# Optimization experiments

Hardware: AMD Instinct MI355X
Metric: run time of the kernel (lower is better)

Reference implementation:

```python
import jax, jax.numpy as jnp
import numpy as np

B, S, H, NH = 4, 2048, 768, 12
HD = H // NH

def _ln(x, g, b, eps=1e-5):
    m = jnp.mean(x, -1, keepdims=True)
    v = jnp.mean((x - m) ** 2, -1, keepdims=True)
    return (x - m) * jax.lax.rsqrt(v + eps) * g + b

def setup_inputs() -> dict:
    key = jax.random.key(0)
    ks = jax.random.split(key, 16)
    s = 0.02
    return {
        "x": jax.random.normal(ks[0], (B, S, H), jnp.float32),
        "prev_state": jax.random.normal(ks[1], (B, S, H), jnp.float32),
        "mask": jax.random.randint(ks[2], (B,), 0, 2).astype(bool),
        # depthwise conv1d (groups=H, k=3): torch weight [H, 1, 3] == OIH
        "conv_dw_w": jax.random.normal(ks[3], (H, 1, 3), jnp.float32) * s,
        "conv_dw_b": jnp.zeros((H,), jnp.float32),
        # pointwise conv1d (k=1) stored as [out, in]
        "conv_pw_w": jax.random.normal(ks[4], (H, H), jnp.float32) * s,
        "conv_pw_b": jnp.zeros((H,), jnp.float32),
        "cn_g": jnp.ones((H,), jnp.float32), "cn_b": jnp.zeros((H,), jnp.float32),
        "Wq": jax.random.normal(ks[5], (H, H), jnp.float32) * s, "bq": jnp.zeros((H,), jnp.float32),
        "Wk": jax.random.normal(ks[6], (H, H), jnp.float32) * s, "bk": jnp.zeros((H,), jnp.float32),
        "Wv": jax.random.normal(ks[7], (H, H), jnp.float32) * s, "bv": jnp.zeros((H,), jnp.float32),
        "Wo": jax.random.normal(ks[8], (H, H), jnp.float32) * s, "bo": jnp.zeros((H,), jnp.float32),
        "pn_g": jnp.ones((H,), jnp.float32), "pn_b": jnp.zeros((H,), jnp.float32),
        "Wpost": jax.random.normal(ks[9], (H, H), jnp.float32) * s, "bpost": jnp.zeros((H,), jnp.float32),
        "Wg": jax.random.normal(ks[10], (1, 2 * H), jnp.float32) * s, "bg": jnp.zeros((1,), jnp.float32),
    }

def reference(x, prev_state, mask, conv_dw_w, conv_dw_b, conv_pw_w, conv_pw_b,
              cn_g, cn_b, Wq, bq, Wk, bk, Wv, bv, Wo, bo,
              pn_g, pn_b, Wpost, bpost, Wg, bg):
    # ---- bridge: depthwise conv (k=3) -> pointwise conv (k=1) -> GELU -> LN ----
    mem_t = prev_state.transpose(0, 2, 1)  # [B, H, S]
    dw = jax.lax.conv_general_dilated(
        mem_t, conv_dw_w, window_strides=(1,), padding=[(1, 1)],
        feature_group_count=H, dimension_numbers=("NCH", "OIH", "NCH")) + conv_dw_b[None, :, None]
    pw = jnp.einsum("bhs,oh->bos", dw, conv_pw_w) + conv_pw_b[None, :, None]
    bridged = jax.nn.gelu(pw, approximate=False).transpose(0, 2, 1)  # [B, S, H]
    bridged = _ln(bridged, cn_g, cn_b)
    # ---- cross attention: q from x, k/v from bridged memory (nope, non-causal) ----
    q = (jnp.einsum("bsh,oh->bso", x, Wq) + bq).reshape(B, S, NH, HD)
    k = (jnp.einsum("bsh,oh->bso", bridged, Wk) + bk).reshape(B, S, NH, HD)
    v = (jnp.einsum("bsh,oh->bso", bridged, Wv) + bv).reshape(B, S, NH, HD)
    scores = jnp.einsum("bqnd,bknd->bnqk", q, k) / np.float32(np.sqrt(HD))
    attn = jax.nn.softmax(scores, axis=-1)
    ao = jnp.einsum("bnqk,bknd->bqnd", attn, v).reshape(B, S, H)
    ao = jnp.einsum("bsh,oh->bso", ao, Wo) + bo
    # ---- post-attn norm, linear, gate, scatter-add back under mask ----
    inj = _ln(ao, pn_g, pn_b)
    inj = jnp.einsum("bsh,oh->bso", inj, Wpost) + bpost
    gate = jax.nn.sigmoid(jnp.einsum("bsh,oh->bso", jnp.concatenate([x, bridged], -1), Wg) + bg)
    gated = gate * jnp.tanh(inj)
    mf = mask.astype(x.dtype)[:, None, None]  # batch-row select == masked scatter-add
    out = x + mf * gated
    # masked MSE aux loss (only over selected rows, as in the original)
    denom = jnp.maximum(mask.sum(), 1).astype(x.dtype) * np.float32(S * H)
    aux = jnp.sum(mf * (bridged - x) ** 2) / denom
    return out, aux
```

## Files before the change

kernel.cpp:

```cpp
#include <hip/hip_runtime.h>
#include <math.h>

#define B_ 4
#define S_ 2048
#define H_ 768
#define NH_ 12
#define HD_ 64
#define BSH (B_ * S_ * H_)
#define NROWS (B_ * S_)
#define WSZ (H_ * H_)

typedef __attribute__((ext_vector_type(8))) short bf16x8;
typedef __attribute__((ext_vector_type(4))) short s16x4;
typedef __attribute__((ext_vector_type(4))) float f32x4;
typedef __attribute__((ext_vector_type(2))) unsigned u32x2;
typedef __attribute__((ext_vector_type(4))) unsigned u32x4;

__device__ __forceinline__ short f2bf(float f) {
  union { float f; unsigned u; } x; x.f = f;
  unsigned r = x.u + 0x7FFF + ((x.u >> 16) & 1);
  return (short)(r >> 16);
}
__device__ __forceinline__ float bf2f(short s) {
  union { unsigned u; float f; } x;
  x.u = ((unsigned)(unsigned short)s) << 16;
  return x.f;
}
__device__ __forceinline__ unsigned bfpack(float lo, float hi) {
  union { float f; unsigned u; } a, b; a.f = lo; b.f = hi;
  return __builtin_amdgcn_perm(b.u, a.u, 0x07060302);
}

__device__ __forceinline__ float fexp2(float x) {
#if __has_builtin(__builtin_amdgcn_exp2f)
  return __builtin_amdgcn_exp2f(x);
#else
  float r;
  asm("v_exp_f32 %0, %1" : "=v"(r) : "v"(x));
  return r;
#endif
}

__device__ __forceinline__ void plswap32(unsigned& a, unsigned& b) {
#if __has_builtin(__builtin_amdgcn_permlane32_swap)
  u32x2 r = __builtin_amdgcn_permlane32_swap(a, b, false, false);
  a = r.x; b = r.y;
#else
  asm volatile("v_permlane32_swap_b32 %0, %1" : "+v"(a), "+v"(b));
#endif
}
__device__ __forceinline__ void plswap16(unsigned& a, unsigned& b) {
#if __has_builtin(__builtin_amdgcn_permlane16_swap)
  u32x2 r = __builtin_amdgcn_permlane16_swap(a, b, false, false);
  a = r.x; b = r.y;
#else
  asm volatile("v_permlane16_swap_b32 %0, %1" : "+v"(a), "+v"(b));
#endif
}

typedef __attribute__((address_space(1))) const unsigned int g_u32;
typedef __attribute__((address_space(3))) unsigned int l_u32;
__device__ __forceinline__ void gload16(const void* g, void* l) {
  __builtin_amdgcn_global_load_lds((g_u32*)g, (l_u32*)l, 16, 0, 0);
}

__global__ __launch_bounds__(256) void cvt_x_k(const float* __restrict__ src,
                                               short* __restrict__ dst) {
  int i = (blockIdx.x * 256 + threadIdx.x) * 4;
  float4 v = *(const float4*)(src + i);
  s16x4 o = {f2bf(v.x), f2bf(v.y), f2bf(v.z), f2bf(v.w)};
  *(s16x4*)(dst + i) = o;
}

__global__ __launch_bounds__(256) void cvt6_k(const float* w0, const float* w1,
                                              const float* w2, const float* w3,
                                              const float* w4, const float* w5,
                                              short* __restrict__ dst) {
  int i = (blockIdx.x * 256 + threadIdx.x) * 4;
  int m = i / WSZ;
  int off = i - m * WSZ;
  const float* s = m == 0 ? w0 : m == 1 ? w1 : m == 2 ? w2 : m == 3 ? w3 : m == 4 ? w4 : w5;
  float sc = (m == 1) ? 0.1803368802f : 1.0f;
  float4 v = *(const float4*)(s + off);
  s16x4 o = {f2bf(v.x * sc), f2bf(v.y * sc), f2bf(v.z * sc), f2bf(v.w * sc)};
  *(s16x4*)(dst + i) = o;
}

__global__ __launch_bounds__(192) void dwconv_k(const float* __restrict__ prev,
                                                const float* __restrict__ w3,
                                                const float* __restrict__ bias,
                                                short* __restrict__ out) {
  int row = blockIdx.x;
  int s = row & (S_ - 1);
  int h = threadIdx.x * 4;
  size_t base = (size_t)row * H_ + h;
  float4 c = *(const float4*)(prev + base);
  float4 wa = *(const float4*)(w3 + h * 3);
  float4 wb = *(const float4*)(w3 + h * 3 + 4);
  float4 wc = *(const float4*)(w3 + h * 3 + 8);
  float4 bi = *(const float4*)(bias + h);
  float4 acc;
  acc.x = bi.x + c.x * wa.y;
  acc.y = bi.y + c.y * wb.x;
  acc.z = bi.z + c.z * wb.w;
  acc.w = bi.w + c.w * wc.z;
  if (s > 0) {
    float4 l = *(const float4*)(prev + base - H_);
    acc.x += l.x * wa.x; acc.y += l.y * wa.w; acc.z += l.z * wb.z; acc.w += l.w * wc.y;
  }
  if (s < S_ - 1) {
    float4 r = *(const float4*)(prev + base + H_);
    acc.x += r.x * wa.z; acc.y += r.y * wb.y; acc.z += r.z * wc.x; acc.w += r.w * wc.w;
  }
  s16x4 o = {f2bf(acc.x), f2bf(acc.y), f2bf(acc.z), f2bf(acc.w)};
  *(s16x4*)(out + base) = o;
}

struct GemmJob {
  const short* A; const short* W; const float* bias; short* C; int act; int tout;
  float bscale;
};

__global__ __launch_bounds__(256, 2) void gemm_bf2(GemmJob j0, GemmJob j1, GemmJob j2) {
  int d = blockIdx.x;
  int z = d / 384, r5 = d - z * 384;
  GemmJob j = z == 0 ? j0 : (z == 1 ? j1 : j2);
  int xcd = r5 & 7, s5 = r5 >> 3;
  int nx = s5 % 6, ny = xcd + 8 * (s5 / 6);
  __shared__ short As[3][128 * 64];
  __shared__ short Ws[2][128 * 64];
  int tid = threadIdx.x, lane = tid & 63, w = tid >> 6;
  int wr = w >> 1, wc = w & 1, lm = lane & 15, lq = lane >> 4;
  int lm7 = lm & 15 & 7;
  int rb8 = (lq ^ lm7) << 3, rb8x = rb8 ^ 32;
  int m0 = ny * 128, n0 = nx * 128;
  int srow = lane >> 3;
  int jl = ((lane & 7) ^ srow) * 8;
  const short* gA = j.A + (size_t)(m0 + w * 32 + srow) * H_ + jl;
  const short* gW = j.W + (size_t)(n0 + w * 32 + srow) * H_ + jl;
  int lbase = w * 2048;

  f32x4 acc[4][4];
#pragma unroll
  for (int i = 0; i < 4; ++i)
#pragma unroll
    for (int jj = 0; jj < 4; ++jj) acc[i][jj] = (f32x4){0.f, 0.f, 0.f, 0.f};

#pragma unroll
  for (int c = 0; c < 4; ++c)
    gload16(gA + (size_t)(c * 8) * H_, &As[0][lbase + c * 512]);
#pragma unroll
  for (int c = 0; c < 4; ++c)
    gload16(gW + (size_t)(c * 8) * H_, &Ws[0][lbase + c * 512]);
#pragma unroll
  for (int c = 0; c < 4; ++c)
    gload16(gA + 64 + (size_t)(c * 8) * H_, &As[1][lbase + c * 512]);

  const int NST = H_ / 64;
  for (int t = 0; t < NST; ++t) {
    if (t < NST - 1) asm volatile("s_waitcnt vmcnt(4)" ::: "memory");
    else             asm volatile("s_waitcnt vmcnt(0)" ::: "memory");
    __builtin_amdgcn_s_barrier();
    __builtin_amdgcn_sched_barrier(0);
    if (t + 1 < NST) {
      int kt1 = (t + 1) * 64;
#pragma unroll
      for (int c = 0; c < 4; ++c)
        gload16(gW + kt1 + (size_t)(c * 8) * H_, &Ws[(t + 1) & 1][lbase + c * 512]);
    }
    if (t + 2 < NST) {
      int kt2 = (t + 2) * 64;
      int a2 = (t + 2) % 3;
#pragma unroll
      for (int c = 0; c < 4; ++c)
        gload16(gA + kt2 + (size_t)(c * 8) * H_, &As[a2][lbase + c * 512]);
    }
    const short* Aw = &As[t % 3][0];
    const short* Ww = &Ws[t & 1][0];
#pragma unroll
    for (int kk = 0; kk < 2; ++kk) {
      int ro = kk ? rb8x : rb8;
      bf16x8 af[4], wf[4];
#pragma unroll
      for (int i = 0; i < 4; ++i)
        af[i] = *(const bf16x8*)&Aw[(wr * 64 + i * 16 + lm) * 64 + ro];
#pragma unroll
      for (int jj = 0; jj < 4; ++jj)
        wf[jj] = *(const bf16x8*)&Ww[(wc * 64 + jj * 16 + lm) * 64 + ro];
#pragma unroll
      for (int i = 0; i < 4; ++i)
#pragma unroll
        for (int jj = 0; jj < 4; ++jj)
          acc[i][jj] = __builtin_amdgcn_mfma_f32_16x16x32_bf16(af[i], wf[jj], acc[i][jj], 0, 0, 0);
    }
  }

  if (!j.tout) {
#pragma unroll
    for (int jj = 0; jj < 4; ++jj) {
      int col = n0 + wc * 64 + jj * 16 + lm;
      float bn = j.bias[col] * j.bscale;
#pragma unroll
      for (int i = 0; i < 4; ++i) {
        int mrow = m0 + wr * 64 + i * 16 + lq * 4;
#pragma unroll
        for (int r = 0; r < 4; ++r) {
          float cv = acc[i][jj][r] + bn;
          if (j.act) cv = 0.5f * cv * (1.0f + erff(cv * 0.70710678118f));
          j.C[(size_t)(mrow + r) * H_ + col] = f2bf(cv);
        }
      }
    }
  } else {
    int b = m0 >> 11;
    int sb = (m0 & (S_ - 1)) + wr * 64;
#pragma unroll
    for (int jj = 0; jj < 4; ++jj) {
      int col = n0 + wc * 64 + jj * 16 + lm;
      float bn = j.bias[col] * j.bscale;
      short* cp = j.C + ((size_t)(b * H_ + col)) * S_;
#pragma unroll
      for (int i = 0; i < 4; ++i) {
        int s = sb + i * 16 + lq * 4;
        s16x4 pk = {f2bf(acc[i][jj][0] + bn), f2bf(acc[i][jj][1] + bn),
                    f2bf(acc[i][jj][2] + bn), f2bf(acc[i][jj][3] + bn)};
        *(s16x4*)(cp + s) = pk;
      }
    }
  }
}

__global__ __launch_bounds__(256, 3) void gemm_n64(const short* __restrict__ A,
                                                   const short* __restrict__ W,
                                                   const float* __restrict__ bias,
                                                   short* __restrict__ C, int act) {
  int d = blockIdx.x;
  int xcd = d & 7, s5 = d >> 3;
  int nx = s5 % 12, ny = xcd + 8 * (s5 / 12);
  __shared__ short As[2][128 * 64];
  __shared__ short Ws[2][64 * 64];
  int tid = threadIdx.x, lane = tid & 63, w = tid >> 6;
  int wm = w >> 1, wn = w & 1, lm = lane & 15, lq = lane >> 4;
  int lm7 = lm & 7;
  int rb8 = (lq ^ lm7) << 3, rb8x = rb8 ^ 32;
  int m0 = ny * 128, n0 = nx * 64;
  int srow = lane >> 3;
  int jl = ((lane & 7) ^ srow) * 8;
  const short* gA = A + (size_t)(m0 + w * 32 + srow) * H_ + jl;
  const short* gW = W + (size_t)(n0 + w * 16 + srow) * H_ + jl;
  int lbaseA = w * 2048;
  int lbaseW = w * 1024;

  f32x4 acc[4][2];
#pragma unroll
  for (int i = 0; i < 4; ++i)
#pragma unroll
    for (int jj = 0; jj < 2; ++jj) acc[i][jj] = (f32x4){0.f, 0.f, 0.f, 0.f};

#pragma unroll
  for (int c = 0; c < 4; ++c)
    gload16(gA + (size_t)(c * 8) * H_, &As[0][lbaseA + c * 512]);
#pragma unroll
  for (int c = 0; c < 2; ++c)
    gload16(gW + (size_t)(c * 8) * H_, &Ws[0][lbaseW + c * 512]);

  for (int kt = 0, pb = 0; kt < H_; kt += 64, pb ^= 1) {
    __syncthreads();
    if (kt + 64 < H_) {
#pragma unroll
      for (int c = 0; c < 4; ++c)
        gload16(gA + kt + 64 + (size_t)(c * 8) * H_, &As[pb ^ 1][lbaseA + c * 512]);
#pragma unroll
      for (int c = 0; c < 2; ++c)
        gload16(gW + kt + 64 + (size_t)(c * 8) * H_, &Ws[pb ^ 1][lbaseW + c * 512]);
    }
    const short* Aw = &As[pb][0];
    const short* Ww = &Ws[pb][0];
#pragma unroll
    for (int kk = 0; kk < 2; ++kk) {
      int ro = kk ? rb8x : rb8;
      bf16x8 af[4], wf[2];
#pragma unroll
      for (int i = 0; i < 4; ++i)
        af[i] = *(const bf16x8*)&Aw[(wm * 64 + i * 16 + lm) * 64 + ro];
#pragma unroll
      for (int jj = 0; jj < 2; ++jj)
        wf[jj] = *(const bf16x8*)&Ww[(wn * 32 + jj * 16 + lm) * 64 + ro];
#pragma unroll
      for (int i = 0; i < 4; ++i)
#pragma unroll
        for (int jj = 0; jj < 2; ++jj)
          acc[i][jj] = __builtin_amdgcn_mfma_f32_16x16x32_bf16(af[i], wf[jj], acc[i][jj], 0, 0, 0);
    }
  }

#pragma unroll
  for (int jj = 0; jj < 2; ++jj) {
    int col = n0 + wn * 32 + jj * 16 + lm;
    float bn = bias[col];
#pragma unroll
    for (int i = 0; i < 4; ++i) {
      int mrow = m0 + wm * 64 + i * 16 + lq * 4;
#pragma unroll
      for (int r = 0; r < 4; ++r) {
        float cv = acc[i][jj][r] + bn;
        if (act) cv = 0.5f * cv * (1.0f + erff(cv * 0.70710678118f));
        C[(size_t)(mrow + r) * H_ + col] = f2bf(cv);
      }
    }
  }
}

__global__ __launch_bounds__(256) void ln_bf(const short* __restrict__ X,
                                             short* __restrict__ Y,
                                             const float* __restrict__ g,
                                             const float* __restrict__ bb) {
  int row = blockIdx.x;
  size_t base = (size_t)row * H_;
  int h0 = threadIdx.x, h1 = h0 + 256, h2 = h0 + 512;
  float x0 = bf2f(X[base + h0]), x1 = bf2f(X[base + h1]), x2 = bf2f(X[base + h2]);
  float s = x0 + x1 + x2;
  float s2 = x0 * x0 + x1 * x1 + x2 * x2;
  for (int off = 32; off > 0; off >>= 1) {
    s += __shfl_down(s, off);
    s2 += __shfl_down(s2, off);
  }
  __shared__ float sa[4], sq[4], st[2];
  int wid = threadIdx.x >> 6, lane = threadIdx.x & 63;
  if (lane == 0) { sa[wid] = s; sq[wid] = s2; }
  __syncthreads();
  if (threadIdx.x == 0) {
    float ts = sa[0] + sa[1] + sa[2] + sa[3];
    float ts2 = sq[0] + sq[1] + sq[2] + sq[3];
    float mean = ts * (1.0f / H_);
    float var = ts2 * (1.0f / H_) - mean * mean;
    st[0] = mean;
    st[1] = rsqrtf(var + 1e-5f);
  }
  __syncthreads();
  float mean = st[0], rstd = st[1];
  Y[base + h0] = f2bf((x0 - mean) * rstd * g[h0] + bb[h0]);
  Y[base + h1] = f2bf((x1 - mean) * rstd * g[h1] + bb[h1]);
  Y[base + h2] = f2bf((x2 - mean) * rstd * g[h2] + bb[h2]);
}

__global__ __launch_bounds__(256, 3) void attn8_k(const short* __restrict__ qb,
                                                  const short* __restrict__ kb,
                                                  const short* __restrict__ vtb,
                                                  short* __restrict__ aob) {
  __shared__ short Ks[2][64 * 64];
  __shared__ short Vt[2][64 * 64];
  int tid = threadIdx.x, lane = tid & 63, w = tid >> 6;
  int lm = lane & 15, lq = lane >> 4;
  int lm7 = lm & 7;
  int dd = blockIdx.x;
  int xcd = dd & 7, slot = dd >> 3;
  int g = xcd + 8 * (slot >> 4);
  int qx = slot & 15;
  int b = g / NH_, n = g - b * NH_;
  int q0 = qx * 128;
  int hoff = n * HD_;

  int rb8 = (lq ^ lm7) << 3;
  int rb8x = rb8 ^ 32;

  bf16x8 qf[2][2];
#pragma unroll
  for (int qg = 0; qg < 2; ++qg) {
    const short* qrow = qb + ((size_t)(b * S_ + q0 + w * 32 + qg * 16 + lm)) * H_ + hoff;
    qf[qg][0] = *(const bf16x8*)(qrow + lq * 8);
    qf[qg][1] = *(const bf16x8*)(qrow + 32 + lq * 8);
  }

  bf16x8 onef = {0x3F80, 0x3F80, 0x3F80, 0x3F80, 0x3F80, 0x3F80, 0x3F80, 0x3F80};
  f32x4 ls[2];
  ls[0] = (f32x4){0.f, 0.f, 0.f, 0.f};
  ls[1] = (f32x4){0.f, 0.f, 0.f, 0.f};

  f32x4 o[4][2];
#pragma unroll
  for (int i = 0; i < 4; ++i)
#pragma unroll
    for (int qg = 0; qg < 2; ++qg) o[i][qg] = (f32x4){0.f, 0.f, 0.f, 0.f};

  int jl = ((lane & 7) ^ (lane >> 3)) * 8;
  int rr = w * 16 + (lane >> 3);
  const short* kgl = kb + ((size_t)(b * S_ + rr)) * H_ + hoff + jl;
  const short* vgl = vtb + ((size_t)(b * H_ + hoff + rr)) * S_ + jl;
  int lbase = w * 1024;

#pragma unroll
  for (int c = 0; c < 2; ++c) {
    gload16(kgl + (size_t)(c * 8) * H_, &Ks[0][lbase + c * 512]);
    gload16(vgl + (size_t)(c * 8) * S_, &Vt[0][lbase + c * 512]);
  }

  for (int kt = 0, pb = 0; kt < S_; kt += 64, pb ^= 1) {
    __syncthreads();
    if (kt + 64 < S_) {
#pragma unroll
      for (int c = 0; c < 2; ++c) {
        gload16(kgl + (size_t)(kt + 64 + c * 8) * H_, &Ks[pb ^ 1][lbase + c * 512]);
        gload16(vgl + (size_t)(c * 8) * S_ + (kt + 64), &Vt[pb ^ 1][lbase + c * 512]);
      }
    }
    const short* Kw = &Ks[pb][0];
    const short* Vw = &Vt[pb][0];

    f32x4 st[4][2];
    __builtin_amdgcn_s_setprio(1);
#pragma unroll
    for (int ni = 0; ni < 4; ++ni) {
      int krow = (ni * 16 + lm) * 64;
      bf16x8 ka0 = *(const bf16x8*)&Kw[krow + rb8];
      bf16x8 ka1 = *(const bf16x8*)&Kw[krow + rb8x];
#pragma unroll
      for (int qg = 0; qg < 2; ++qg) {
        f32x4 z = (f32x4){0.f, 0.f, 0.f, 0.f};
        z = __builtin_amdgcn_mfma_f32_16x16x32_bf16(ka0, qf[qg][0], z, 0, 0, 0);
        st[ni][qg] = __builtin_amdgcn_mfma_f32_16x16x32_bf16(ka1, qf[qg][1], z, 0, 0, 0);
      }
    }
    __builtin_amdgcn_s_setprio(0);

    bf16x8 pf[2][2];
#pragma unroll
    for (int qg = 0; qg < 2; ++qg) {
      unsigned pw0, pw1, pw2, pw3, pw4, pw5, pw6, pw7;
      {
        float p0 = fexp2(st[0][qg][0]), p1 = fexp2(st[0][qg][1]);
        float p2 = fexp2(st[0][qg][2]), p3 = fexp2(st[0][qg][3]);
        pw0 = bfpack(p0, p1); pw1 = bfpack(p2, p3);
      }
      {
        float p0 = fexp2(st[1][qg][0]), p1 = fexp2(st[1][qg][1]);
        float p2 = fexp2(st[1][qg][2]), p3 = fexp2(st[1][qg][3]);
        pw2 = bfpack(p0, p1); pw3 = bfpack(p2, p3);
      }
      {
        float p0 = fexp2(st[2][qg][0]), p1 = fexp2(st[2][qg][1]);
        float p2 = fexp2(st[2][qg][2]), p3 = fexp2(st[2][qg][3]);
        pw4 = bfpack(p0, p1); pw5 = bfpack(p2, p3);
      }
      {
        float p0 = fexp2(st[3][qg][0]), p1 = fexp2(st[3][qg][1]);
        float p2 = fexp2(st[3][qg][2]), p3 = fexp2(st[3][qg][3]);
        pw6 = bfpack(p0, p1); pw7 = bfpack(p2, p3);
      }
      plswap32(pw0, pw2); plswap16(pw0, pw2);
      plswap32(pw1, pw3); plswap16(pw1, pw3);
      plswap32(pw4, pw6); plswap16(pw4, pw6);
      plswap32(pw5, pw7); plswap16(pw5, pw7);
      union { u32x4 u; bf16x8 v; } c0u, c1u;
      c0u.u = (u32x4){pw0, pw1, pw2, pw3};
      c1u.u = (u32x4){pw4, pw5, pw6, pw7};
      pf[qg][0] = c0u.v;
      pf[qg][1] = c1u.v;
    }

    __builtin_amdgcn_s_setprio(1);
#pragma unroll
    for (int qg = 0; qg < 2; ++qg) {
      ls[qg] = __builtin_amdgcn_mfma_f32_16x16x32_bf16(onef, pf[qg][0], ls[qg], 0, 0, 0);
      ls[qg] = __builtin_amdgcn_mfma_f32_16x16x32_bf16(onef, pf[qg][1], ls[qg], 0, 0, 0);
    }
#pragma unroll
    for (int nd = 0; nd < 4; ++nd) {
      int vrow = (nd * 16 + lm) * 64;
      bf16x8 va0 = *(const bf16x8*)&Vw[vrow + rb8];
      bf16x8 va1 = *(const bf16x8*)&Vw[vrow + rb8x];
#pragma unroll
      for (int qg = 0; qg < 2; ++qg) {
        o[nd][qg] = __builtin_amdgcn_mfma_f32_16x16x32_bf16(va0, pf[qg][0], o[nd][qg], 0, 0, 0);
        o[nd][qg] = __builtin_amdgcn_mfma_f32_16x16x32_bf16(va1, pf[qg][1], o[nd][qg], 0, 0, 0);
      }
    }
    __builtin_amdgcn_s_setprio(0);
  }

#pragma unroll
  for (int qg = 0; qg < 2; ++qg) {
    float inv = 1.0f / ls[qg][0];
    short* orow = aob + ((size_t)(b * S_ + q0 + w * 32 + qg * 16 + lm)) * H_ + hoff;
#pragma unroll
    for (int nd = 0; nd < 4; ++nd) {
      s16x4 pk = {f2bf(o[nd][qg][0] * inv), f2bf(o[nd][qg][1] * inv),
                  f2bf(o[nd][qg][2] * inv), f2bf(o[nd][qg][3] * inv)};
      *(s16x4*)(orow + nd * 16 + lq * 4) = pk;
    }
  }
}

__global__ __launch_bounds__(192) void gate_out_k(const float* __restrict__ x,
                                                  const short* __restrict__ br,
                                                  const short* __restrict__ inj,
                                                  const int* __restrict__ mask,
                                                  const float* __restrict__ Wg,
                                                  const float* __restrict__ bg,
                                                  float* __restrict__ out,
                                                  float* __restrict__ paux) {
  int row = blockIdx.x;
  int b = row >> 11;
  size_t base = (size_t)row * H_;
  int h = threadIdx.x * 4;
  float4 xv = *(const float4*)(x + base + h);
  s16x4 brv = *(const s16x4*)(br + base + h);
  s16x4 inv = *(const s16x4*)(inj + base + h);
  float4 wg0 = *(const float4*)(Wg + h);
  float4 wg1 = *(const float4*)(Wg + H_ + h);
  float b0 = bf2f(brv.x), b1 = bf2f(brv.y), b2 = bf2f(brv.z), b3 = bf2f(brv.w);
  float dot = xv.x * wg0.x + xv.y * wg0.y + xv.z * wg0.z + xv.w * wg0.w
            + b0 * wg1.x + b1 * wg1.y + b2 * wg1.z + b3 * wg1.w;
  float d0 = b0 - xv.x, d1 = b1 - xv.y, d2 = b2 - xv.z, d3 = b3 - xv.w;
  float aux = d0 * d0 + d1 * d1 + d2 * d2 + d3 * d3;
  for (int off = 32; off > 0; off >>= 1) {
    dot += __shfl_down(dot, off);
    aux += __shfl_down(aux, off);
  }
  __shared__ float sd[3], sx[3], gsh[2];
  int wid = threadIdx.x >> 6, lane = threadIdx.x & 63;
  if (lane == 0) { sd[wid] = dot; sx[wid] = aux; }
  __syncthreads();
  if (threadIdx.x == 0) {
    float td = sd[0] + sd[1] + sd[2];
    float ta = sx[0] + sx[1] + sx[2];
    gsh[0] = 1.0f / (1.0f + expf(-(td + bg[0])));
    gsh[1] = ta;
  }
  __syncthreads();
  float mf = (mask[b] != 0) ? 1.0f : 0.0f;
  float gm = gsh[0] * mf;
  float v0 = bf2f(inv.x), v1 = bf2f(inv.y), v2 = bf2f(inv.z), v3 = bf2f(inv.w);
  float e0 = __expf(2.f * v0), e1 = __expf(2.f * v1), e2 = __expf(2.f * v2), e3 = __expf(2.f * v3);
  float4 ov;
  ov.x = xv.x + gm * ((e0 - 1.f) / (e0 + 1.f));
  ov.y = xv.y + gm * ((e1 - 1.f) / (e1 + 1.f));
  ov.z = xv.z + gm * ((e2 - 1.f) / (e2 + 1.f));
  ov.w = xv.w + gm * ((e3 - 1.f) / (e3 + 1.f));
  *(float4*)(out + base + h) = ov;
  if (threadIdx.x == 0) paux[row] = mf * gsh[1];
}

__global__ __launch_bounds__(256) void aux_reduce_k(const float* __restrict__ paux,
                                                    const int* __restrict__ mask,
                                                    float* __restrict__ outp) {
  float s = 0.f;
  for (int i = threadIdx.x; i < NROWS; i += 256) s += paux[i];
  for (int off = 32; off > 0; off >>= 1) s += __shfl_down(s, off);
  __shared__ float sw[4];
  int wid = threadIdx.x >> 6, lane = threadIdx.x & 63;
  if (lane == 0) sw[wid] = s;
  __syncthreads();
  if (threadIdx.x == 0) {
    float t = sw[0] + sw[1] + sw[2] + sw[3];
    int nm = (mask[0] != 0) + (mask[1] != 0) + (mask[2] != 0) + (mask[3] != 0);
    if (nm < 1) nm = 1;
    outp[0] = t / ((float)nm * (float)(S_ * H_));
  }
}

extern "C" void kernel_launch(void* const* d_in, const int* in_sizes, int n_in,
                              void* d_out, int out_size, void* d_ws, size_t ws_size,
                              hipStream_t stream) {
  const float* x     = (const float*)d_in[0];
  const float* prev  = (const float*)d_in[1];
  const int*   mask  = (const int*)d_in[2];
  const float* dw_w  = (const float*)d_in[3];
  const float* dw_b  = (const float*)d_in[4];
  const float* pw_w  = (const float*)d_in[5];
  const float* pw_b  = (const float*)d_in[6];
  const float* cn_g  = (const float*)d_in[7];
  const float* cn_b  = (const float*)d_in[8];
  const float* Wq    = (const float*)d_in[9];
  const float* bq    = (const float*)d_in[10];
  const float* Wk    = (const float*)d_in[11];
  const float* bk    = (const float*)d_in[12];
  const float* Wv    = (const float*)d_in[13];
  const float* bv    = (const float*)d_in[14];
  const float* Wo    = (const float*)d_in[15];
  const float* bo    = (const float*)d_in[16];
  const float* pn_g  = (const float*)d_in[17];
  const float* pn_b  = (const float*)d_in[18];
  const float* Wpost = (const float*)d_in[19];
  const float* bpost = (const float*)d_in[20];
  const float* Wg    = (const float*)d_in[21];
  const float* bg    = (const float*)d_in[22];
  float* out = (float*)d_out;

  short* B0 = (short*)d_ws;
  short* B1 = B0 + BSH;
  short* B2 = B1 + BSH;
  short* B3 = B2 + BSH;
  short* B4 = B3 + BSH;
  short* B5 = B4 + BSH;
  short* WW = B5 + BSH;
  float* paux = (float*)(WW + 6 * WSZ);

  const float C1 = 0.1803368802f;

  GemmJob jq = {B0, WW + WSZ,     bq, B1, 0, 0, C1};
  GemmJob jk = {B3, WW + 2 * WSZ, bk, B4, 0, 0, 1.0f};
  GemmJob jv = {B3, WW + 3 * WSZ, bv, B5, 0, 1, 1.0f};

  cvt6_k<<<6 * WSZ / 1024, 256, 0, stream>>>(pw_w, Wq, Wk, Wv, Wo, Wpost, WW);
  cvt_x_k<<<BSH / 1024, 256, 0, stream>>>(x, B0);
  dwconv_k<<<NROWS, 192, 0, stream>>>(prev, dw_w, dw_b, B1);
  gemm_n64<<<768, 256, 0, stream>>>(B1, WW, pw_b, B2, 1);
  ln_bf<<<NROWS, 256, 0, stream>>>(B2, B3, cn_g, cn_b);
  gemm_bf2<<<1152, 256, 0, stream>>>(jq, jk, jv);
  attn8_k<<<768, 256, 0, stream>>>(B1, B4, B5, B2);
  gemm_n64<<<768, 256, 0, stream>>>(B2, WW + 4 * WSZ, bo, B4, 0);
  ln_bf<<<NROWS, 256, 0, stream>>>(B4, B4, pn_g, pn_b);
  gemm_n64<<<768, 256, 0, stream>>>(B4, WW + 5 * WSZ, bpost, B5, 0);
  gate_out_k<<<NROWS, 192, 0, stream>>>(x, B3, B5, mask, Wg, bg, out, paux);
  aux_reduce_k<<<1, 256, 0, stream>>>(paux, mask, out + BSH);
}
```

Measured before the change: 358.9 us.

## Software-pipeline attention loop so PV MFMAs overlap next tile's QK and exp

Restructures the attention inner loop into a prologue, a steady state and an epilogue. Each iteration computes QK scores for the current tile while issuing the row-sum and PV MFMAs for the previous tile's probabilities. The exp/pack work and V fragment loads follow in the same iteration. The goal is to hide exp latency and LDS reads behind matrix-core work. In exchange it holds more live registers (pf, va, st across iterations), which could cause spills or lower occupancy, and the buffer reuse across the shifted stages needs careful barrier correctness.

```diff
diff --git a/kernel.cpp b/kernel.cpp
--- a/kernel.cpp
+++ b/kernel.cpp
@@ -131,7 +131,7 @@
   __shared__ short Ws[2][128 * 64];
   int tid = threadIdx.x, lane = tid & 63, w = tid >> 6;
   int wr = w >> 1, wc = w & 1, lm = lane & 15, lq = lane >> 4;
-  int lm7 = lm & 15 & 7;
+  int lm7 = lm & 7;
   int rb8 = (lq ^ lm7) << 3, rb8x = rb8 ^ 32;
   int m0 = ny * 128, n0 = nx * 128;
   int srow = lane >> 3;
@@ -344,7 +344,7 @@
   Y[base + h2] = f2bf((x2 - mean) * rstd * g[h2] + bb[h2]);
 }
 
-__global__ __launch_bounds__(256, 3) void attn8_k(const short* __restrict__ qb,
+__global__ __launch_bounds__(256, 3) void attn9_k(const short* __restrict__ qb,
                                                   const short* __restrict__ kb,
                                                   const short* __restrict__ vtb,
                                                   short* __restrict__ aob) {
@@ -389,31 +389,82 @@
   const short* vgl = vtb + ((size_t)(b * H_ + hoff + rr)) * S_ + jl;
   int lbase = w * 1024;
 
+  bf16x8 pf[2][2];
+  bf16x8 va[4][2];
+  f32x4 st[4][2];
+
 #pragma unroll
   for (int c = 0; c < 2; ++c) {
     gload16(kgl + (size_t)(c * 8) * H_, &Ks[0][lbase + c * 512]);
     gload16(vgl + (size_t)(c * 8) * S_, &Vt[0][lbase + c * 512]);
   }
-
-  for (int kt = 0, pb = 0; kt < S_; kt += 64, pb ^= 1) {
+  __syncthreads();
+#pragma unroll
+  for (int c = 0; c < 2; ++c) {
+    gload16(kgl + (size_t)(64 + c * 8) * H_, &Ks[1][lbase + c * 512]);
+    gload16(vgl + (size_t)(c * 8) * S_ + 64, &Vt[1][lbase + c * 512]);
+  }
+
+  __builtin_amdgcn_s_setprio(1);
+#pragma unroll
+  for (int ni = 0; ni < 4; ++ni) {
+    int krow = (ni * 16 + lm) * 64;
+    bf16x8 ka0 = *(const bf16x8*)&Ks[0][krow + rb8];
+    bf16x8 ka1 = *(const bf16x8*)&Ks[0][krow + rb8x];
+#pragma unroll
+    for (int qg = 0; qg < 2; ++qg) {
+      f32x4 z = (f32x4){0.f, 0.f, 0.f, 0.f};
+      z = __builtin_amdgcn_mfma_f32_16x16x32_bf16(ka0, qf[qg][0], z, 0, 0, 0);
+      st[ni][qg] = __builtin_amdgcn_mfma_f32_16x16x32_bf16(ka1, qf[qg][1], z, 0, 0, 0);
+    }
+  }
+  __builtin_amdgcn_s_setprio(0);
+#pragma unroll
+  for (int qg = 0; qg < 2; ++qg) {
+    unsigned pw0, pw1, pw2, pw3, pw4, pw5, pw6, pw7;
+    pw0 = bfpack(fexp2(st[0][qg][0]), fexp2(st[0][qg][1]));
+    pw1 = bfpack(fexp2(st[0][qg][2]), fexp2(st[0][qg][3]));
+    pw2 = bfpack(fexp2(st[1][qg][0]), fexp2(st[1][qg][1]));
+    pw3 = bfpack(fexp2(st[1][qg][2]), fexp2(st[1][qg][3]));
+    pw4 = bfpack(fexp2(st[2][qg][0]), fexp2(st[2][qg][1]));
+    pw5 = bfpack(fexp2(st[2][qg][2]), fexp2(st[2][qg][3]));
+    pw6 = bfpack(fexp2(st[3][qg][0]), fexp2(st[3][qg][1]));
+    pw7 = bfpack(fexp2(st[3][qg][2]), fexp2(st[3][qg][3]));
+    plswap32(pw0, pw2); plswap16(pw0, pw2);
+    plswap32(pw1, pw3); plswap16(pw1, pw3);
+    plswap32(pw4, pw6); plswap16(pw4, pw6);
+    plswap32(pw5, pw7); plswap16(pw5, pw7);
+    union { u32x4 u; bf16x8 v; } c0u, c1u;
+    c0u.u = (u32x4){pw0, pw1, pw2, pw3};
+    c1u.u = (u32x4){pw4, pw5, pw6, pw7};
+    pf[qg][0] = c0u.v;
+    pf[qg][1] = c1u.v;
+  }
+#pragma unroll
+  for (int nd = 0; nd < 4; ++nd) {
+    int vrow = (nd * 16 + lm) * 64;
+    va[nd][0] = *(const bf16x8*)&Vt[0][vrow + rb8];
+    va[nd][1] = *(const bf16x8*)&Vt[0][vrow + rb8x];
+  }
+
+  for (int t = 1; t < S_ / 64; ++t) {
+    int pb = t & 1;
     __syncthreads();
-    if (kt + 64 < S_) {
+    if (t + 1 < S_ / 64) {
+      int kt1 = (t + 1) * 64;
 #pragma unroll
       for (int c = 0; c < 2; ++c) {
-        gload16(kgl + (size_t)(kt + 64 + c * 8) * H_, &Ks[pb ^ 1][lbase + c * 512]);
-        gload16(vgl + (size_t)(c * 8) * S_ + (kt + 64), &Vt[pb ^ 1][lbase + c * 512]);
+        gload16(kgl + (size_t)(kt1 + c * 8) * H_, &Ks[pb ^ 1][lbase + c * 512]);
+        gload16(vgl + (size_t)(c * 8) * S_ + kt1, &Vt[pb ^ 1][lbase + c * 512]);
       }
     }
-    const short* Kw = &Ks[pb][0];
-    const short* Vw = &Vt[pb][0];
-
-    f32x4 st[4][2];
+
     __builtin_amdgcn_s_setprio(1);
 #pragma unroll
     for (int ni = 0; ni < 4; ++ni) {
       int krow = (ni * 16 + lm) * 64;
-      bf16x8 ka0 = *(const bf16x8*)&Kw[krow + rb8];
-      bf16x8 ka1 = *(const bf16x8*)&Kw[krow + rb8x];
+      bf16x8 ka0 = *(const bf16x8*)&Ks[pb][krow + rb8];
+      bf16x8 ka1 = *(const bf16x8*)&Ks[pb][krow + rb8x];
 #pragma unroll
       for (int qg = 0; qg < 2; ++qg) {
         f32x4 z = (f32x4){0.f, 0.f, 0.f, 0.f};
@@ -421,32 +472,31 @@
         st[ni][qg] = __builtin_amdgcn_mfma_f32_16x16x32_bf16(ka1, qf[qg][1], z, 0, 0, 0);
       }
     }
+#pragma unroll
+    for (int qg = 0; qg < 2; ++qg) {
+      ls[qg] = __builtin_amdgcn_mfma_f32_16x16x32_bf16(onef, pf[qg][0], ls[qg], 0, 0, 0);
+      ls[qg] = __builtin_amdgcn_mfma_f32_16x16x32_bf16(onef, pf[qg][1], ls[qg], 0, 0, 0);
+    }
+#pragma unroll
+    for (int nd = 0; nd < 4; ++nd)
+#pragma unroll
+      for (int qg = 0; qg < 2; ++qg) {
+        o[nd][qg] = __builtin_amdgcn_mfma_f32_16x16x32_bf16(va[nd][0], pf[qg][0], o[nd][qg], 0, 0, 0);
+        o[nd][qg] = __builtin_amdgcn_mfma_f32_16x16x32_bf16(va[nd][1], pf[qg][1], o[nd][qg], 0, 0, 0);
+      }
     __builtin_amdgcn_s_setprio(0);
 
-    bf16x8 pf[2][2];
 #pragma unroll
     for (int qg = 0; qg < 2; ++qg) {
       unsigned pw0, pw1, pw2, pw3, pw4, pw5, pw6, pw7;
-      {
-        float p0 = fexp2(st[0][qg][0]), p1 = fexp2(st[0][qg][1]);
-        float p2 = fexp2(st[0][qg][2]), p3 = fexp2(st[0][qg][3]);
-        pw0 = bfpack(p0, p1); pw1 = bfpack(p2, p3);
-      }
-      {
-        float p0 = fexp2(st[1][qg][0]), p1 = fexp2(st[1][qg][1]);
-        float p2 = fexp2(st[1][qg][2]), p3 = fexp2(st[1][qg][3]);
-        pw2 = bfpack(p0, p1); pw3 = bfpack(p2, p3);
-      }
-      {
-        float p0 = fexp2(st[2][qg][0]), p1 = fexp2(st[2][qg][1]);
-        float p2 = fexp2(st[2][qg][2]), p3 = fexp2(st[2][qg][3]);
-        pw4 = bfpack(p0, p1); pw5 = bfpack(p2, p3);
-      }
-      {
-        float p0 = fexp2(st[3][qg][0]), p1 = fexp2(st[3][qg][1]);
-        float p2 = fexp2(st[3][qg][2]), p3 = fexp2(st[3][qg][3]);
-        pw6 = bfpack(p0, p1); pw7 = bfpack(p2, p3);
-      }
+      pw0 = bfpack(fexp2(st[0][qg][0]), fexp2(st[0][qg][1]));
+      pw1 = bfpack(fexp2(st[0][qg][2]), fexp2(st[0][qg][3]));
+      pw2 = bfpack(fexp2(st[1][qg][0]), fexp2(st[1][qg][1]));
+      pw3 = bfpack(fexp2(st[1][qg][2]), fexp2(st[1][qg][3]));
+      pw4 = bfpack(fexp2(st[2][qg][0]), fexp2(st[2][qg][1]));
+      pw5 = bfpack(fexp2(st[2][qg][2]), fexp2(st[2][qg][3]));
+      pw6 = bfpack(fexp2(st[3][qg][0]), fexp2(st[3][qg][1]));
+      pw7 = bfpack(fexp2(st[3][qg][2]), fexp2(st[3][qg][3]));
       plswap32(pw0, pw2); plswap16(pw0, pw2);
       plswap32(pw1, pw3); plswap16(pw1, pw3);
       plswap32(pw4, pw6); plswap16(pw4, pw6);
@@ -457,26 +507,28 @@
       pf[qg][0] = c0u.v;
       pf[qg][1] = c1u.v;
     }
-
-    __builtin_amdgcn_s_setprio(1);
-#pragma unroll
-    for (int qg = 0; qg < 2; ++qg) {
-      ls[qg] = __builtin_amdgcn_mfma_f32_16x16x32_bf16(onef, pf[qg][0], ls[qg], 0, 0, 0);
-      ls[qg] = __builtin_amdgcn_mfma_f32_16x16x32_bf16(onef, pf[qg][1], ls[qg], 0, 0, 0);
-    }
 #pragma unroll
     for (int nd = 0; nd < 4; ++nd) {
       int vrow = (nd * 16 + lm) * 64;
-      bf16x8 va0 = *(const bf16x8*)&Vw[vrow + rb8];
-      bf16x8 va1 = *(const bf16x8*)&Vw[vrow + rb8x];
-#pragma unroll
-      for (int qg = 0; qg < 2; ++qg) {
-        o[nd][qg] = __builtin_amdgcn_mfma_f32_16x16x32_bf16(va0, pf[qg][0], o[nd][qg], 0, 0, 0);
-        o[nd][qg] = __builtin_amdgcn_mfma_f32_16x16x32_bf16(va1, pf[qg][1], o[nd][qg], 0, 0, 0);
-      }
-    }
-    __builtin_amdgcn_s_setprio(0);
-  }
+      va[nd][0] = *(const bf16x8*)&Vt[pb][vrow + rb8];
+      va[nd][1] = *(const bf16x8*)&Vt[pb][vrow + rb8x];
+    }
+  }
+
+  __builtin_amdgcn_s_setprio(1);
+#pragma unroll
+  for (int qg = 0; qg < 2; ++qg) {
+    ls[qg] = __builtin_amdgcn_mfma_f32_16x16x32_bf16(onef, pf[qg][0], ls[qg], 0, 0, 0);
+    ls[qg] = __builtin_amdgcn_mfma_f32_16x16x32_bf16(onef, pf[qg][1], ls[qg], 0, 0, 0);
+  }
+#pragma unroll
+  for (int nd = 0; nd < 4; ++nd)
+#pragma unroll
+    for (int qg = 0; qg < 2; ++qg) {
+      o[nd][qg] = __builtin_amdgcn_mfma_f32_16x16x32_bf16(va[nd][0], pf[qg][0], o[nd][qg], 0, 0, 0);
+      o[nd][qg] = __builtin_amdgcn_mfma_f32_16x16x32_bf16(va[nd][1], pf[qg][1], o[nd][qg], 0, 0, 0);
+    }
+  __builtin_amdgcn_s_setprio(0);
 
 #pragma unroll
   for (int qg = 0; qg < 2; ++qg) {
@@ -608,7 +660,7 @@
   gemm_n64<<<768, 256, 0, stream>>>(B1, WW, pw_b, B2, 1);
   ln_bf<<<NROWS, 256, 0, stream>>>(B2, B3, cn_g, cn_b);
   gemm_bf2<<<1152, 256, 0, stream>>>(jq, jk, jv);
-  attn8_k<<<768, 256, 0, stream>>>(B1, B4, B5, B2);
+  attn9_k<<<768, 256, 0, stream>>>(B1, B4, B5, B2);
   gemm_n64<<<768, 256, 0, stream>>>(B2, WW + 4 * WSZ, bo, B4, 0);
   ln_bf<<<NROWS, 256, 0, stream>>>(B4, B4, pn_g, pn_b);
   gemm_n64<<<768, 256, 0, stream>>>(B4, WW + 5 * WSZ, bpost, B5, 0);
```

New measurement: 352.7 us, median of 2. About the same (-1.7%).

## Restructure attention kernel to 8 waves with software-pipelined softmax and PV

Applied to the files above, without the earlier changes.

The attention kernel moves from 4 waves each owning 32 query rows to 8 waves each owning 16, so every wave uses half the registers and more waves fit per CU. The loop is software-pipelined: QK^T for the current tile is issued alongside PV for the previous tile's probabilities, which are kept in a triple-buffered V shared-memory ring. The aim is to overlap exp/pack VALU work with MFMA and raise occupancy. In exchange each K/V tile is reused by fewer query rows per wave, and the kernel gains more barriers per block.

```diff
diff --git a/kernel.cpp b/kernel.cpp
--- a/kernel.cpp
+++ b/kernel.cpp
@@ -131,7 +131,7 @@
   __shared__ short Ws[2][128 * 64];
   int tid = threadIdx.x, lane = tid & 63, w = tid >> 6;
   int wr = w >> 1, wc = w & 1, lm = lane & 15, lq = lane >> 4;
-  int lm7 = lm & 15 & 7;
+  int lm7 = lm & 7;
   int rb8 = (lq ^ lm7) << 3, rb8x = rb8 ^ 32;
   int m0 = ny * 128, n0 = nx * 128;
   int srow = lane >> 3;
@@ -344,12 +344,12 @@
   Y[base + h2] = f2bf((x2 - mean) * rstd * g[h2] + bb[h2]);
 }
 
-__global__ __launch_bounds__(256, 3) void attn8_k(const short* __restrict__ qb,
-                                                  const short* __restrict__ kb,
-                                                  const short* __restrict__ vtb,
-                                                  short* __restrict__ aob) {
+__global__ __launch_bounds__(512, 6) void attn10_k(const short* __restrict__ qb,
+                                                   const short* __restrict__ kb,
+                                                   const short* __restrict__ vtb,
+                                                   short* __restrict__ aob) {
   __shared__ short Ks[2][64 * 64];
-  __shared__ short Vt[2][64 * 64];
+  __shared__ short Vt[3][64 * 64];
   int tid = threadIdx.x, lane = tid & 63, w = tid >> 6;
   int lm = lane & 15, lq = lane >> 4;
   int lm7 = lm & 7;
@@ -364,89 +364,108 @@
   int rb8 = (lq ^ lm7) << 3;
   int rb8x = rb8 ^ 32;
 
-  bf16x8 qf[2][2];
-#pragma unroll
-  for (int qg = 0; qg < 2; ++qg) {
-    const short* qrow = qb + ((size_t)(b * S_ + q0 + w * 32 + qg * 16 + lm)) * H_ + hoff;
-    qf[qg][0] = *(const bf16x8*)(qrow + lq * 8);
-    qf[qg][1] = *(const bf16x8*)(qrow + 32 + lq * 8);
+  bf16x8 qf0, qf1;
+  {
+    const short* qrow = qb + ((size_t)(b * S_ + q0 + w * 16 + lm)) * H_ + hoff;
+    qf0 = *(const bf16x8*)(qrow + lq * 8);
+    qf1 = *(const bf16x8*)(qrow + 32 + lq * 8);
   }
 
   bf16x8 onef = {0x3F80, 0x3F80, 0x3F80, 0x3F80, 0x3F80, 0x3F80, 0x3F80, 0x3F80};
-  f32x4 ls[2];
-  ls[0] = (f32x4){0.f, 0.f, 0.f, 0.f};
-  ls[1] = (f32x4){0.f, 0.f, 0.f, 0.f};
-
-  f32x4 o[4][2];
-#pragma unroll
-  for (int i = 0; i < 4; ++i)
-#pragma unroll
-    for (int qg = 0; qg < 2; ++qg) o[i][qg] = (f32x4){0.f, 0.f, 0.f, 0.f};
-
-  int jl = ((lane & 7) ^ (lane >> 3)) * 8;
-  int rr = w * 16 + (lane >> 3);
-  const short* kgl = kb + ((size_t)(b * S_ + rr)) * H_ + hoff + jl;
-  const short* vgl = vtb + ((size_t)(b * H_ + hoff + rr)) * S_ + jl;
-  int lbase = w * 1024;
-
-#pragma unroll
-  for (int c = 0; c < 2; ++c) {
-    gload16(kgl + (size_t)(c * 8) * H_, &Ks[0][lbase + c * 512]);
-    gload16(vgl + (size_t)(c * 8) * S_, &Vt[0][lbase + c * 512]);
-  }
-
-  for (int kt = 0, pb = 0; kt < S_; kt += 64, pb ^= 1) {
+  f32x4 ls = (f32x4){0.f, 0.f, 0.f, 0.f};
+  f32x4 o[4];
+#pragma unroll
+  for (int i = 0; i < 4; ++i) o[i] = (f32x4){0.f, 0.f, 0.f, 0.f};
+
+  int r0 = tid >> 3;
+  int jl = ((tid & 7) ^ (r0 & 7)) * 8;
+  const short* kgl = kb + ((size_t)(b * S_ + r0)) * H_ + hoff + jl;
+  const short* vgl = vtb + ((size_t)(b * H_ + hoff + r0)) * S_ + jl;
+  int lbase = w * 512;
+
+  bf16x8 pf0, pf1;
+  f32x4 st[4];
+
+  gload16(kgl, &Ks[0][lbase]);
+  gload16(vgl, &Vt[0][lbase]);
+  __syncthreads();
+  gload16(kgl + (size_t)64 * H_, &Ks[1][lbase]);
+  gload16(vgl + 64, &Vt[1][lbase]);
+
+  __builtin_amdgcn_s_setprio(1);
+#pragma unroll
+  for (int ni = 0; ni < 4; ++ni) {
+    int krow = (ni * 16 + lm) * 64;
+    bf16x8 ka0 = *(const bf16x8*)&Ks[0][krow + rb8];
+    bf16x8 ka1 = *(const bf16x8*)&Ks[0][krow + rb8x];
+    f32x4 z = (f32x4){0.f, 0.f, 0.f, 0.f};
+    z = __builtin_amdgcn_mfma_f32_16x16x32_bf16(ka0, qf0, z, 0, 0, 0);
+    st[ni] = __builtin_amdgcn_mfma_f32_16x16x32_bf16(ka1, qf1, z, 0, 0, 0);
+  }
+  __builtin_amdgcn_s_setprio(0);
+  {
+    unsigned pw0, pw1, pw2, pw3, pw4, pw5, pw6, pw7;
+    pw0 = bfpack(fexp2(st[0][0]), fexp2(st[0][1]));
+    pw1 = bfpack(fexp2(st[0][2]), fexp2(st[0][3]));
+    pw2 = bfpack(fexp2(st[1][0]), fexp2(st[1][1]));
+    pw3 = bfpack(fexp2(st[1][2]), fexp2(st[1][3]));
+    pw4 = bfpack(fexp2(st[2][0]), fexp2(st[2][1]));
+    pw5 = bfpack(fexp2(st[2][2]), fexp2(st[2][3]));
+    pw6 = bfpack(fexp2(st[3][0]), fexp2(st[3][1]));
+    pw7 = bfpack(fexp2(st[3][2]), fexp2(st[3][3]));
+    plswap32(pw0, pw2); plswap16(pw0, pw2);
+    plswap32(pw1, pw3); plswap16(pw1, pw3);
+    plswap32(pw4, pw6); plswap16(pw4, pw6);
+    plswap32(pw5, pw7); plswap16(pw5, pw7);
+    union { u32x4 u; bf16x8 v; } c0u, c1u;
+    c0u.u = (u32x4){pw0, pw1, pw2, pw3};
+    c1u.u = (u32x4){pw4, pw5, pw6, pw7};
+    pf0 = c0u.v;
+    pf1 = c1u.v;
+  }
+
+  int vprv = 0, vcur = 1, vnxt = 2;
+  for (int t = 1; t < S_ / 64; ++t) {
+    int kb2 = t & 1;
     __syncthreads();
-    if (kt + 64 < S_) {
-#pragma unroll
-      for (int c = 0; c < 2; ++c) {
-        gload16(kgl + (size_t)(kt + 64 + c * 8) * H_, &Ks[pb ^ 1][lbase + c * 512]);
-        gload16(vgl + (size_t)(c * 8) * S_ + (kt + 64), &Vt[pb ^ 1][lbase + c * 512]);
-      }
-    }
-    const short* Kw = &Ks[pb][0];
-    const short* Vw = &Vt[pb][0];
-
-    f32x4 st[4][2];
+    if (t + 1 < S_ / 64) {
+      int kt1 = (t + 1) * 64;
+      gload16(kgl + (size_t)kt1 * H_, &Ks[kb2 ^ 1][lbase]);
+      gload16(vgl + kt1, &Vt[vnxt][lbase]);
+    }
+
     __builtin_amdgcn_s_setprio(1);
 #pragma unroll
     for (int ni = 0; ni < 4; ++ni) {
       int krow = (ni * 16 + lm) * 64;
-      bf16x8 ka0 = *(const bf16x8*)&Kw[krow + rb8];
-      bf16x8 ka1 = *(const bf16x8*)&Kw[krow + rb8x];
-#pragma unroll
-      for (int qg = 0; qg < 2; ++qg) {
-        f32x4 z = (f32x4){0.f, 0.f, 0.f, 0.f};
-        z = __builtin_amdgcn_mfma_f32_16x16x32_bf16(ka0, qf[qg][0], z, 0, 0, 0);
-        st[ni][qg] = __builtin_amdgcn_mfma_f32_16x16x32_bf16(ka1, qf[qg][1], z, 0, 0, 0);
-      }
+      bf16x8 ka0 = *(const bf16x8*)&Ks[kb2][krow + rb8];
+      bf16x8 ka1 = *(const bf16x8*)&Ks[kb2][krow + rb8x];
+      f32x4 z = (f32x4){0.f, 0.f, 0.f, 0.f};
+      z = __builtin_amdgcn_mfma_f32_16x16x32_bf16(ka0, qf0, z, 0, 0, 0);
+      st[ni] = __builtin_amdgcn_mfma_f32_16x16x32_bf16(ka1, qf1, z, 0, 0, 0);
+    }
+    ls = __builtin_amdgcn_mfma_f32_16x16x32_bf16(onef, pf0, ls, 0, 0, 0);
+    ls = __builtin_amdgcn_mfma_f32_16x16x32_bf16(onef, pf1, ls, 0, 0, 0);
+#pragma unroll
+    for (int nd = 0; nd < 4; ++nd) {
+      int vrow = (nd * 16 + lm) * 64;
+      bf16x8 va0 = *(const bf16x8*)&Vt[vprv][vrow + rb8];
+      bf16x8 va1 = *(const bf16x8*)&Vt[vprv][vrow + rb8x];
+      o[nd] = __builtin_amdgcn_mfma_f32_16x16x32_bf16(va0, pf0, o[nd], 0, 0, 0);
+      o[nd] = __builtin_amdgcn_mfma_f32_16x16x32_bf16(va1, pf1, o[nd], 0, 0, 0);
     }
     __builtin_amdgcn_s_setprio(0);
 
-    bf16x8 pf[2][2];
-#pragma unroll
-    for (int qg = 0; qg < 2; ++qg) {
+    {
       unsigned pw0, pw1, pw2, pw3, pw4, pw5, pw6, pw7;
-      {
-        float p0 = fexp2(st[0][qg][0]), p1 = fexp2(st[0][qg][1]);
-        float p2 = fexp2(st[0][qg][2]), p3 = fexp2(st[0][qg][3]);
-        pw0 = bfpack(p0, p1); pw1 = bfpack(p2, p3);
-      }
-      {
-        float p0 = fexp2(st[1][qg][0]), p1 = fexp2(st[1][qg][1]);
-        float p2 = fexp2(st[1][qg][2]), p3 = fexp2(st[1][qg][3]);
-        pw2 = bfpack(p0, p1); pw3 = bfpack(p2, p3);
-      }
-      {
-        float p0 = fexp2(st[2][qg][0]), p1 = fexp2(st[2][qg][1]);
-        float p2 = fexp2(st[2][qg][2]), p3 = fexp2(st[2][qg][3]);
-        pw4 = bfpack(p0, p1); pw5 = bfpack(p2, p3);
-      }
-      {
-        float p0 = fexp2(st[3][qg][0]), p1 = fexp2(st[3][qg][1]);
-        float p2 = fexp2(st[3][qg][2]), p3 = fexp2(st[3][qg][3]);
-        pw6 = bfpack(p0, p1); pw7 = bfpack(p2, p3);
-      }
+      pw0 = bfpack(fexp2(st[0][0]), fexp2(st[0][1]));
+      pw1 = bfpack(fexp2(st[0][2]), fexp2(st[0][3]));
+      pw2 = bfpack(fexp2(st[1][0]), fexp2(st[1][1]));
+      pw3 = bfpack(fexp2(st[1][2]), fexp2(st[1][3]));
+      pw4 = bfpack(fexp2(st[2][0]), fexp2(st[2][1]));
+      pw5 = bfpack(fexp2(st[2][2]), fexp2(st[2][3]));
+      pw6 = bfpack(fexp2(st[3][0]), fexp2(st[3][1]));
+      pw7 = bfpack(fexp2(st[3][2]), fexp2(st[3][3]));
       plswap32(pw0, pw2); plswap16(pw0, pw2);
       plswap32(pw1, pw3); plswap16(pw1, pw3);
       plswap32(pw4, pw6); plswap16(pw4, pw6);
@@ -454,38 +473,33 @@
       union { u32x4 u; bf16x8 v; } c0u, c1u;
       c0u.u = (u32x4){pw0, pw1, pw2, pw3};
       c1u.u = (u32x4){pw4, pw5, pw6, pw7};
-      pf[qg][0] = c0u.v;
-      pf[qg][1] = c1u.v;
-    }
-
-    __builtin_amdgcn_s_setprio(1);
-#pragma unroll
-    for (int qg = 0; qg < 2; ++qg) {
-      ls[qg] = __builtin_amdgcn_mfma_f32_16x16x32_bf16(onef, pf[qg][0], ls[qg], 0, 0, 0);
-      ls[qg] = __builtin_amdgcn_mfma_f32_16x16x32_bf16(onef, pf[qg][1], ls[qg], 0, 0, 0);
-    }
+      pf0 = c0u.v;
+      pf1 = c1u.v;
+    }
+
+    int tmp = vprv; vprv = vcur; vcur = vnxt; vnxt = tmp;
+  }
+
+  __builtin_amdgcn_s_setprio(1);
+  ls = __builtin_amdgcn_mfma_f32_16x16x32_bf16(onef, pf0, ls, 0, 0, 0);
+  ls = __builtin_amdgcn_mfma_f32_16x16x32_bf16(onef, pf1, ls, 0, 0, 0);
+#pragma unroll
+  for (int nd = 0; nd < 4; ++nd) {
+    int vrow = (nd * 16 + lm) * 64;
+    bf16x8 va0 = *(const bf16x8*)&Vt[vprv][vrow + rb8];
+    bf16x8 va1 = *(const bf16x8*)&Vt[vprv][vrow + rb8x];
+    o[nd] = __builtin_amdgcn_mfma_f32_16x16x32_bf16(va0, pf0, o[nd], 0, 0, 0);
+    o[nd] = __builtin_amdgcn_mfma_f32_16x16x32_bf16(va1, pf1, o[nd], 0, 0, 0);
+  }
+  __builtin_amdgcn_s_setprio(0);
+
+  {
+    float inv = 1.0f / ls[0];
+    short* orow = aob + ((size_t)(b * S_ + q0 + w * 16 + lm)) * H_ + hoff;
 #pragma unroll
     for (int nd = 0; nd < 4; ++nd) {
-      int vrow = (nd * 16 + lm) * 64;
-      bf16x8 va0 = *(const bf16x8*)&Vw[vrow + rb8];
-      bf16x8 va1 = *(const bf16x8*)&Vw[vrow + rb8x];
-#pragma unroll
-      for (int qg = 0; qg < 2; ++qg) {
-        o[nd][qg] = __builtin_amdgcn_mfma_f32_16x16x32_bf16(va0, pf[qg][0], o[nd][qg], 0, 0, 0);
-        o[nd][qg] = __builtin_amdgcn_mfma_f32_16x16x32_bf16(va1, pf[qg][1], o[nd][qg], 0, 0, 0);
-      }
-    }
-    __builtin_amdgcn_s_setprio(0);
-  }
-
-#pragma unroll
-  for (int qg = 0; qg < 2; ++qg) {
-    float inv = 1.0f / ls[qg][0];
-    short* orow = aob + ((size_t)(b * S_ + q0 + w * 32 + qg * 16 + lm)) * H_ + hoff;
-#pragma unroll
-    for (int nd = 0; nd < 4; ++nd) {
-      s16x4 pk = {f2bf(o[nd][qg][0] * inv), f2bf(o[nd][qg][1] * inv),
-                  f2bf(o[nd][qg][2] * inv), f2bf(o[nd][qg][3] * inv)};
+      s16x4 pk = {f2bf(o[nd][0] * inv), f2bf(o[nd][1] * inv),
+                  f2bf(o[nd][2] * inv), f2bf(o[nd][3] * inv)};
       *(s16x4*)(orow + nd * 16 + lq * 4) = pk;
     }
   }
@@ -608,7 +622,7 @@
   gemm_n64<<<768, 256, 0, stream>>>(B1, WW, pw_b, B2, 1);
   ln_bf<<<NROWS, 256, 0, stream>>>(B2, B3, cn_g, cn_b);
   gemm_bf2<<<1152, 256, 0, stream>>>(jq, jk, jv);
-  attn8_k<<<768, 256, 0, stream>>>(B1, B4, B5, B2);
+  attn10_k<<<768, 512, 0, stream>>>(B1, B4, B5, B2);
   gemm_n64<<<768, 256, 0, stream>>>(B2, WW + 4 * WSZ, bo, B4, 0);
   ln_bf<<<NROWS, 256, 0, stream>>>(B4, B4, pn_g, pn_b);
   gemm_n64<<<768, 256, 0, stream>>>(B4, WW + 5 * WSZ, bpost, B5, 0);
```

Result: no change. 361.1 us (+0.6%).
